# Kernel optimization log

Hardware: AMD Instinct MI355X
Metric: run time of the kernel (lower is better)

The kernel has to match this reference:

```python
import jax, jax.numpy as jnp
import numpy as np

N = 100_000      # nodes
E = 1_600_000    # edges (before self loops)
IN = 128         # in_dim
HID = 64         # hidden_dim (per head)
HEADS = 2
NEG_SLOPE = 0.2  # PyG GATConv default negative_slope


def setup_inputs() -> dict:
    key = jax.random.key(0)
    k = jax.random.split(key, 6)
    x = jax.random.normal(k[0], (N, IN), jnp.float32)
    edge_index = jax.random.randint(k[1], (2, E), 0, N, dtype=jnp.int64)
    # GATConv linear (no bias in lin, bias added after aggregation in PyG)
    W = jax.random.normal(k[2], (IN, HEADS * HID), jnp.float32) * (1.0 / np.sqrt(IN))
    att_src = jax.random.normal(k[3], (HEADS, HID), jnp.float32) * 0.1
    att_dst = jax.random.normal(k[4], (HEADS, HID), jnp.float32) * 0.1
    bias = jnp.zeros((HEADS * HID,), jnp.float32)
    prelu_w = jnp.full((HEADS * HID,), 0.25, jnp.float32)  # nn.PReLU default init
    return {"x": x, "edge_index": edge_index, "W": W, "att_src": att_src,
            "att_dst": att_dst, "bias": bias, "prelu_w": prelu_w}


def reference(x, edge_index, W, att_src, att_dst, bias, prelu_w):
    n = x.shape[0]
    h = (x @ W).reshape(n, HEADS, HID)                 # [N,H,C]
    a_s = jnp.einsum('nhc,hc->nh', h, att_src)         # [N,H]
    a_d = jnp.einsum('nhc,hc->nh', h, att_dst)         # [N,H]
    # add self loops (PyG default add_self_loops=True)
    loops = jnp.arange(n, dtype=edge_index.dtype)
    src = jnp.concatenate([edge_index[0], loops])      # [Et]
    dst = jnp.concatenate([edge_index[1], loops])      # [Et]
    logits = a_s[src] + a_d[dst]                       # [Et,H]
    logits = jnp.where(logits >= 0, logits, NEG_SLOPE * logits)  # LeakyReLU
    # segment softmax over destination neighborhoods
    m = jax.ops.segment_max(logits, dst, num_segments=n)         # [N,H]
    e = jnp.exp(logits - m[dst])
    s = jax.ops.segment_sum(e, dst, num_segments=n)              # [N,H]
    alpha = e / (s[dst] + 1e-16)                                 # [Et,H]
    # (attention dropout p=0.2 is identity in eval mode)
    msg = h[src] * alpha[..., None]                    # [Et,H,C]
    out = jax.ops.segment_sum(msg, dst, num_segments=n).reshape(n, HEADS * HID)
    out = out + bias
    # PReLU with per-channel weight
    return jnp.where(out >= 0, out, prelu_w * out)
```

## Files before the change

### kernel.cpp

```cpp
#include <hip/hip_runtime.h>
#include <hip/hip_fp16.h>
#include <cstdint>
#include <cstddef>

#define NEG_SLOPE 0.2f
#define BSH 8
#define BNODES 256
#define CAP 5120

typedef __attribute__((ext_vector_type(8))) short short8v;
typedef __attribute__((ext_vector_type(4))) float f32x4;
typedef __attribute__((ext_vector_type(2))) uint32_t u32x2;

__device__ __forceinline__ uint32_t bf16pair(float a, float b) {
    uint32_t ua = __float_as_uint(a), ub = __float_as_uint(b);
    ua = (ua + 0x7fffu + ((ua >> 16) & 1u)) >> 16;
    ub = (ub + 0x7fffu + ((ub >> 16) & 1u)) >> 16;
    return ua | (ub << 16);
}
__device__ __forceinline__ uint16_t rne16(float f) {
    uint32_t u = __float_as_uint(f);
    return (uint16_t)((u + 0x7fffu + ((u >> 16) & 1u)) >> 16);
}
__device__ __forceinline__ float bflo(uint32_t u) { return __uint_as_float(u << 16); }
__device__ __forceinline__ float bfhi(uint32_t u) { return __uint_as_float(u & 0xffff0000u); }
__device__ __forceinline__ uint32_t packf16(float a, float b) {
    __half2 h = __floats2half2_rn(a, b);
    return *reinterpret_cast<uint32_t*>(&h);
}

__global__ __launch_bounds__(256, 3) void gemm_att(
    const float* __restrict__ x, const float* __restrict__ W,
    const float* __restrict__ att_src, const float* __restrict__ att_dst,
    uint32_t* __restrict__ hb, float* __restrict__ a_s, float* __restrict__ a_d,
    int* __restrict__ gcur, int nb, int n)
{
    constexpr int PW = 136;
    __shared__ unsigned short Wt[128 * PW];
    __shared__ unsigned short Hs[4][16 * PW];
    const int tid  = threadIdx.x;
    const int w    = tid >> 6;
    const int lane = tid & 63;
    const int cl   = lane & 15;
    const int gq   = lane >> 4;
    const int base = blockIdx.x * 64;

    if (blockIdx.x == 0)
        for (int i = tid; i < nb; i += 256) gcur[i] = 0;

    const float4* W4 = (const float4*)W;
#pragma unroll
    for (int i = 0; i < 16; ++i) {
        int idx = tid + i * 256;
        int k = idx >> 5, c0 = (idx & 31) * 4;
        float4 v = W4[idx];
        Wt[(c0 + 0) * PW + k] = rne16(v.x);
        Wt[(c0 + 1) * PW + k] = rne16(v.y);
        Wt[(c0 + 2) * PW + k] = rne16(v.z);
        Wt[(c0 + 3) * PW + k] = rne16(v.w);
    }

    float asr[8], adr[8];
#pragma unroll
    for (int t = 0; t < 8; ++t) {
        asr[t] = att_src[t * 16 + cl];
        adr[t] = att_dst[t * 16 + cl];
    }
    __syncthreads();

    const int rowg = base + w * 16 + cl;
    const int rowc = rowg < n ? rowg : (n - 1);
    const f32x4* xp = (const f32x4*)(x + (size_t)rowc * 128);

    f32x4 acc[8];
#pragma unroll
    for (int t = 0; t < 8; ++t) acc[t] = (f32x4){0.f, 0.f, 0.f, 0.f};

#pragma unroll
    for (int s = 0; s < 4; ++s) {
        int kq = s * 8 + gq * 2;
        f32x4 f0 = __builtin_nontemporal_load(xp + kq);
        f32x4 f1 = __builtin_nontemporal_load(xp + kq + 1);
        union { short8v v; uint32_t d[4]; } A;
        A.d[0] = bf16pair(f0.x, f0.y);
        A.d[1] = bf16pair(f0.z, f0.w);
        A.d[2] = bf16pair(f1.x, f1.y);
        A.d[3] = bf16pair(f1.z, f1.w);
#pragma unroll
        for (int t = 0; t < 8; ++t) {
            union { short8v v; uint4 q; } B;
            B.q = *(const uint4*)&Wt[(t * 16 + cl) * PW + s * 32 + gq * 8];
            acc[t] = __builtin_amdgcn_mfma_f32_16x16x32_bf16(A.v, B.v, acc[t], 0, 0, 0);
        }
    }

    float ps0[4], ps1[4], pd0[4], pd1[4];
#pragma unroll
    for (int r = 0; r < 4; ++r) { ps0[r] = ps1[r] = pd0[r] = pd1[r] = 0.f; }
#pragma unroll
    for (int t = 0; t < 8; ++t) {
#pragma unroll
        for (int r = 0; r < 4; ++r) {
            float v = acc[t][r];
            if (t < 4) { ps0[r] = fmaf(v, asr[t], ps0[r]); pd0[r] = fmaf(v, adr[t], pd0[r]); }
            else       { ps1[r] = fmaf(v, asr[t], ps1[r]); pd1[r] = fmaf(v, adr[t], pd1[r]); }
        }
    }
#pragma unroll
    for (int off = 1; off < 16; off <<= 1) {
#pragma unroll
        for (int r = 0; r < 4; ++r) {
            ps0[r] += __shfl_xor(ps0[r], off);
            ps1[r] += __shfl_xor(ps1[r], off);
            pd0[r] += __shfl_xor(pd0[r], off);
            pd1[r] += __shfl_xor(pd1[r], off);
        }
    }
    if (cl == 0) {
#pragma unroll
        for (int r = 0; r < 4; ++r) {
            int rg = base + w * 16 + gq * 4 + r;
            if (rg < n) {
                a_s[rg * 2 + 0] = ps0[r]; a_s[rg * 2 + 1] = ps1[r];
                a_d[rg * 2 + 0] = pd0[r]; a_d[rg * 2 + 1] = pd1[r];
            }
        }
    }

#pragma unroll
    for (int t = 0; t < 8; ++t) {
#pragma unroll
        for (int r = 0; r < 4; ++r) {
            int row = gq * 4 + r;
            Hs[w][row * PW + t * 16 + cl] = rne16(acc[t][r]);
        }
    }
    __syncthreads();
#pragma unroll
    for (int q = 0; q < 4; ++q) {
        int row = q * 4 + gq;
        int cu  = 4 * cl;
        uint4 v = *(const uint4*)&Hs[w][row * PW + cu * 2];
        int rg = base + w * 16 + row;
        if (rg < n) *(uint4*)&hb[(size_t)rg * 64 + cu] = v;
    }
}

__global__ __launch_bounds__(256) void bucket_scatter(
    const int* __restrict__ src, const int* __restrict__ dst,
    int* __restrict__ gcur, uint32_t* __restrict__ pairs, int e, int nb)
{
    __shared__ int histL[512];
    __shared__ int gbaseL[512];
    const int tid = threadIdx.x;
    const int t0  = blockIdx.x * 4096;

    for (int i = tid; i < nb; i += 256) histL[i] = 0;
    __syncthreads();

    int      myb[16];
    int      myslot[16];
    uint32_t mypk[16];
#pragma unroll 16
    for (int k = 0; k < 16; ++k) {
        int i = t0 + tid + k * 256;
        if (i < e) {
            int s = __builtin_nontemporal_load(src + i);
            int d = __builtin_nontemporal_load(dst + i);
            int b = d >> BSH;
            myb[k]    = b;
            mypk[k]   = (uint32_t)s | ((uint32_t)(d & (BNODES - 1)) << 17);
            myslot[k] = atomicAdd(&histL[b], 1);
        } else myb[k] = -1;
    }
    __syncthreads();
    for (int i = tid; i < nb; i += 256) {
        int c = histL[i];
        gbaseL[i] = c ? atomicAdd(&gcur[i], c) : 0;
    }
    __syncthreads();
#pragma unroll 16
    for (int k = 0; k < 16; ++k) {
        if (myb[k] >= 0) {
            int p = gbaseL[myb[k]] + myslot[k];
            if (p < CAP) pairs[(size_t)myb[k] * CAP + p] = mypk[k];
        }
    }
}

__global__ __launch_bounds__(512) void build_csr(
    const uint32_t* __restrict__ pairs, const int* __restrict__ gcur,
    const float* __restrict__ a_s, const float* __restrict__ a_d,
    uint4* __restrict__ meta, uint2* __restrict__ edges, int n, int nb)
{
    __shared__ uint32_t pl[CAP];
    __shared__ int degL[BNODES], curL[BNODES];
    __shared__ float sumL[BNODES * 2];
    __shared__ float adL[BNODES * 2];
    __shared__ int bscan[512];
    __shared__ int wsum8[8];
    const int b = blockIdx.x, tid = threadIdx.x;
    const int lane = tid & 63, wid = tid >> 6;
    const int nbase = b * BNODES;
    const int nodes = min(BNODES, n - nbase);

    int tot = 0;
    if (tid < nb) {
        int nn = min(BNODES, n - tid * BNODES);
        tot = min(gcur[tid], CAP) + nn;
    }
    int sc = tot;
#pragma unroll
    for (int off = 1; off < 64; off <<= 1) {
        int t = __shfl_up(sc, off);
        if (lane >= off) sc += t;
    }
    if (lane == 63) wsum8[wid] = sc;
    __syncthreads();
    {
        int woff = 0;
#pragma unroll
        for (int k = 0; k < 8; ++k) woff += (k < wid) ? wsum8[k] : 0;
        bscan[tid] = sc + woff;
    }
    if (tid < BNODES) degL[tid] = 1;
    float es0 = 0.f, es1 = 0.f;
    if (tid < nodes) {
        int g = nbase + tid;
        float2 ad = ((const float2*)a_d)[g];
        adL[2 * tid]     = ad.x;
        adL[2 * tid + 1] = ad.y;
        float2 as = ((const float2*)a_s)[g];
        float l0 = as.x + ad.x; l0 = l0 >= 0.f ? l0 : NEG_SLOPE * l0;
        float l1 = as.y + ad.y; l1 = l1 >= 0.f ? l1 : NEG_SLOPE * l1;
        es0 = __expf(l0); es1 = __expf(l1);
        sumL[2 * tid] = es0; sumL[2 * tid + 1] = es1;
    }
    __syncthreads();
    const int C    = min(gcur[b], CAP);
    const int base = bscan[b] - (C + nodes);

    for (int i = tid; i < C; i += 512) {
        uint32_t p = __builtin_nontemporal_load(pairs + (size_t)b * CAP + i);
        pl[i] = p;
        atomicAdd(&degL[p >> 17], 1);
    }
    __syncthreads();

    int v = (tid < nodes) ? degL[tid] : 0;
    int sc2 = v;
#pragma unroll
    for (int off = 1; off < 64; off <<= 1) {
        int t = __shfl_up(sc2, off);
        if (lane >= off) sc2 += t;
    }
    if (lane == 63 && tid < BNODES) wsum8[wid] = sc2;
    __syncthreads();
    int woff2 = 0;
#pragma unroll
    for (int k = 0; k < 4; ++k) woff2 += (k < wid) ? wsum8[k] : 0;
    const int exc = sc2 - v + woff2;

    if (tid < nodes) {
        edges[base + exc] = make_uint2((uint32_t)(nbase + tid), packf16(es0, es1));
        curL[tid] = exc + 1;
    }
    __syncthreads();
    for (int i = tid; i < C; i += 512) {
        uint32_t p  = pl[i];
        int dl  = p >> 17;
        int s   = p & 0x1FFFF;
        float2 as = ((const float2*)a_s)[s];
        float l0 = as.x + adL[2 * dl];     l0 = l0 >= 0.f ? l0 : NEG_SLOPE * l0;
        float l1 = as.y + adL[2 * dl + 1]; l1 = l1 >= 0.f ? l1 : NEG_SLOPE * l1;
        float e0 = __expf(l0), e1 = __expf(l1);
        int pos = atomicAdd(&curL[dl], 1);
        edges[base + pos] = make_uint2((uint32_t)s, packf16(e0, e1));
        atomicAdd(&sumL[2 * dl],     e0);
        atomicAdd(&sumL[2 * dl + 1], e1);
    }
    __syncthreads();
    if (tid < nodes) {
        uint4 m;
        m.x = (uint32_t)(base + exc);
        m.y = (uint32_t)v;
        m.z = __float_as_uint(1.f / (sumL[2 * tid]     + 1e-16f));
        m.w = __float_as_uint(1.f / (sumL[2 * tid + 1] + 1e-16f));
        meta[nbase + tid] = m;
    }
}

__global__ __launch_bounds__(256) void attn_agg(
    const uint32_t* __restrict__ hb, const uint2* __restrict__ edges,
    const uint4* __restrict__ meta,
    const float* __restrict__ bias, const float* __restrict__ prelu_w,
    float* __restrict__ out, int n)
{
    const int gw   = (blockIdx.x * blockDim.x + threadIdx.x) >> 6;
    const int lane = threadIdx.x & 63;
    if (gw >= n) return;
    const uint4 mt  = meta[gw];
    const int start = (int)mt.x;
    const int deg   = (int)mt.y;
    const float inv0 = __uint_as_float(mt.z);
    const float inv1 = __uint_as_float(mt.w);

    if (deg <= 64) {
        int sv = 0; float al0 = 0.f, al1 = 0.f;
        if (lane < deg) {
            u32x2 ed = __builtin_nontemporal_load((const u32x2*)(edges + start + lane));
            sv = (int)ed.x;
            uint32_t ey = ed.y;
            __half2 h2 = *reinterpret_cast<__half2*>(&ey);
            al0 = __half2float(__low2half(h2))  * inv0;
            al1 = __half2float(__high2half(h2)) * inv1;
        }
        const int g = lane >> 4, r = lane & 15;
        float acc[8];
#pragma unroll
        for (int q = 0; q < 8; ++q) acc[q] = 0.f;

        const uint4* hb4 = (const uint4*)hb;
        const int iters = (deg + 15) >> 4;
        for (int jj = 0; jj < iters; ++jj) {
            const int j0 = jj * 16 + g;
            int   s0  = __shfl(sv, j0);
            int   s1  = __shfl(sv, j0 + 4);
            int   s2  = __shfl(sv, j0 + 8);
            int   s3  = __shfl(sv, j0 + 12);
            float A00 = __shfl(al0, j0),      A10 = __shfl(al1, j0);
            float A01 = __shfl(al0, j0 + 4),  A11 = __shfl(al1, j0 + 4);
            float A02 = __shfl(al0, j0 + 8),  A12 = __shfl(al1, j0 + 8);
            float A03 = __shfl(al0, j0 + 12), A13 = __shfl(al1, j0 + 12);
            float Aa = (r < 8) ? A00 : A10;
            float Ab = (r < 8) ? A01 : A11;
            float Ac = (r < 8) ? A02 : A12;
            float Ad = (r < 8) ? A03 : A13;
            uint4 qa = hb4[(size_t)s0 * 16 + r];
            uint4 qb = hb4[(size_t)s1 * 16 + r];
            uint4 qc = hb4[(size_t)s2 * 16 + r];
            uint4 qd = hb4[(size_t)s3 * 16 + r];
            acc[0] = fmaf(Aa, bflo(qa.x), acc[0]); acc[1] = fmaf(Aa, bfhi(qa.x), acc[1]);
            acc[2] = fmaf(Aa, bflo(qa.y), acc[2]); acc[3] = fmaf(Aa, bfhi(qa.y), acc[3]);
            acc[4] = fmaf(Aa, bflo(qa.z), acc[4]); acc[5] = fmaf(Aa, bfhi(qa.z), acc[5]);
            acc[6] = fmaf(Aa, bflo(qa.w), acc[6]); acc[7] = fmaf(Aa, bfhi(qa.w), acc[7]);
            acc[0] = fmaf(Ab, bflo(qb.x), acc[0]); acc[1] = fmaf(Ab, bfhi(qb.x), acc[1]);
            acc[2] = fmaf(Ab, bflo(qb.y), acc[2]); acc[3] = fmaf(Ab, bfhi(qb.y), acc[3]);
            acc[4] = fmaf(Ab, bflo(qb.z), acc[4]); acc[5] = fmaf(Ab, bfhi(qb.z), acc[5]);
            acc[6] = fmaf(Ab, bflo(qb.w), acc[6]); acc[7] = fmaf(Ab, bfhi(qb.w), acc[7]);
            acc[0] = fmaf(Ac, bflo(qc.x), acc[0]); acc[1] = fmaf(Ac, bfhi(qc.x), acc[1]);
            acc[2] = fmaf(Ac, bflo(qc.y), acc[2]); acc[3] = fmaf(Ac, bfhi(qc.y), acc[3]);
            acc[4] = fmaf(Ac, bflo(qc.z), acc[4]); acc[5] = fmaf(Ac, bfhi(qc.z), acc[5]);
            acc[6] = fmaf(Ac, bflo(qc.w), acc[6]); acc[7] = fmaf(Ac, bfhi(qc.w), acc[7]);
            acc[0] = fmaf(Ad, bflo(qd.x), acc[0]); acc[1] = fmaf(Ad, bfhi(qd.x), acc[1]);
            acc[2] = fmaf(Ad, bflo(qd.y), acc[2]); acc[3] = fmaf(Ad, bfhi(qd.y), acc[3]);
            acc[4] = fmaf(Ad, bflo(qd.z), acc[4]); acc[5] = fmaf(Ad, bfhi(qd.z), acc[5]);
            acc[6] = fmaf(Ad, bflo(qd.w), acc[6]); acc[7] = fmaf(Ad, bfhi(qd.w), acc[7]);
        }
#pragma unroll
        for (int q = 0; q < 8; ++q) {
            acc[q] += __shfl_xor(acc[q], 16);
            acc[q] += __shfl_xor(acc[q], 32);
        }
        if (lane < 16) {
            float4 b0 = ((const float4*)bias)[lane * 2];
            float4 b1 = ((const float4*)bias)[lane * 2 + 1];
            float4 p0 = ((const float4*)prelu_w)[lane * 2];
            float4 p1 = ((const float4*)prelu_w)[lane * 2 + 1];
            f32x4 w0, w1;
            w0.x = acc[0] + b0.x; w0.x = w0.x >= 0.f ? w0.x : p0.x * w0.x;
            w0.y = acc[1] + b0.y; w0.y = w0.y >= 0.f ? w0.y : p0.y * w0.y;
            w0.z = acc[2] + b0.z; w0.z = w0.z >= 0.f ? w0.z : p0.z * w0.z;
            w0.w = acc[3] + b0.w; w0.w = w0.w >= 0.f ? w0.w : p0.w * w0.w;
            w1.x = acc[4] + b1.x; w1.x = w1.x >= 0.f ? w1.x : p1.x * w1.x;
            w1.y = acc[5] + b1.y; w1.y = w1.y >= 0.f ? w1.y : p1.y * w1.y;
            w1.z = acc[6] + b1.z; w1.z = w1.z >= 0.f ? w1.z : p1.z * w1.z;
            w1.w = acc[7] + b1.w; w1.w = w1.w >= 0.f ? w1.w : p1.w * w1.w;
            float* op = out + (size_t)gw * 128 + lane * 8;
            __builtin_nontemporal_store(w0, (f32x4*)op);
            __builtin_nontemporal_store(w1, (f32x4*)(op + 4));
        }
    } else {
        float accL = 0.f, accH = 0.f;
        for (int t0 = 0; t0 < deg; t0 += 64) {
            int tt = t0 + lane;
            int sv = 0; float al0 = 0.f, al1 = 0.f;
            if (tt < deg) {
                uint2 ed = edges[start + tt];
                sv = (int)ed.x;
                __half2 h2 = *reinterpret_cast<__half2*>(&ed.y);
                al0 = __half2float(__low2half(h2))  * inv0;
                al1 = __half2float(__high2half(h2)) * inv1;
            }
            int kmax = min(64, deg - t0);
            for (int j = 0; j < kmax; ++j) {
                int   s  = __shfl(sv, j);
                float A0 = __shfl(al0, j);
                float A1 = __shfl(al1, j);
                float A  = (lane < 32) ? A0 : A1;
                uint32_t u = hb[(size_t)s * 64 + lane];
                accL = fmaf(A, bflo(u), accL);
                accH = fmaf(A, bfhi(u), accH);
            }
        }
        float2 bz = ((const float2*)bias)[lane];
        float2 pw = ((const float2*)prelu_w)[lane];
        float o0 = accL + bz.x, o1 = accH + bz.y;
        o0 = o0 >= 0.f ? o0 : pw.x * o0;
        o1 = o1 >= 0.f ? o1 : pw.y * o1;
        float2 rr; rr.x = o0; rr.y = o1;
        ((float2*)out)[(size_t)gw * 64 + lane] = rr;
    }
}

extern "C" void kernel_launch(void* const* d_in, const int* in_sizes, int n_in,
                              void* d_out, int out_size, void* d_ws, size_t ws_size,
                              hipStream_t stream)
{
    const float* x        = (const float*)d_in[0];
    const int*   ei       = (const int*)d_in[1];
    const float* W        = (const float*)d_in[2];
    const float* att_src  = (const float*)d_in[3];
    const float* att_dst  = (const float*)d_in[4];
    const float* bias     = (const float*)d_in[5];
    const float* prelu_w  = (const float*)d_in[6];
    float* out = (float*)d_out;

    const int n = in_sizes[0] / 128;
    const int e = in_sizes[1] / 2;
    const int* srcp = ei;
    const int* dstp = ei + e;
    const int nb = (n + BNODES - 1) / BNODES;

    uint32_t* hb    = (uint32_t*)d_ws;
    uint4*    meta  = (uint4*)(hb + (size_t)n * 64);
    float*    a_s   = (float*)(meta + n);
    float*    a_d   = a_s + (size_t)n * 2;
    int*      gcur  = (int*)(a_d + (size_t)n * 2);
    uint32_t* pairs = (uint32_t*)(gcur + 512);
    uint2*    edges = (uint2*)(pairs + (size_t)nb * CAP);

    gemm_att<<<(n + 63) / 64, 256, 0, stream>>>(x, W, att_src, att_dst,
                                                hb, a_s, a_d, gcur, nb, n);
    bucket_scatter<<<(e + 4095) / 4096, 256, 0, stream>>>(srcp, dstp, gcur, pairs, e, nb);
    build_csr<<<nb, 512, 0, stream>>>(pairs, gcur, a_s, a_d, meta, edges, n, nb);
    attn_agg<<<(n + 3) / 4, 256, 0, stream>>>(hb, edges, meta, bias, prelu_w, out, n);
}
```

Baseline: 160.5 us.

## Merge GEMM and edge bucket scatter into one launch; specialize aggregation by degree

```diff
diff --git a/kernel.cpp b/kernel.cpp
--- a/kernel.cpp
+++ b/kernel.cpp
@@ -29,24 +29,64 @@
     return *reinterpret_cast<uint32_t*>(&h);
 }
 
-__global__ __launch_bounds__(256, 3) void gemm_att(
+__global__ __launch_bounds__(256, 3) void gemm_scatter(
     const float* __restrict__ x, const float* __restrict__ W,
     const float* __restrict__ att_src, const float* __restrict__ att_dst,
     uint32_t* __restrict__ hb, float* __restrict__ a_s, float* __restrict__ a_d,
-    int* __restrict__ gcur, int nb, int n)
+    const int* __restrict__ src, const int* __restrict__ dst,
+    int* __restrict__ gcur, uint32_t* __restrict__ pairs,
+    int e, int nb, int n, int nbs)
 {
     constexpr int PW = 136;
-    __shared__ unsigned short Wt[128 * PW];
-    __shared__ unsigned short Hs[4][16 * PW];
-    const int tid  = threadIdx.x;
+    __shared__ __align__(16) char smem[52224];
+    const int tid = threadIdx.x;
+
+    if (blockIdx.x < nbs) {
+        int* histL  = (int*)smem;
+        int* gbaseL = histL + 512;
+        const int t0 = blockIdx.x * 4096;
+
+        for (int i = tid; i < nb; i += 256) histL[i] = 0;
+        __syncthreads();
+
+        int      myb[16];
+        int      myslot[16];
+        uint32_t mypk[16];
+#pragma unroll 16
+        for (int k = 0; k < 16; ++k) {
+            int i = t0 + tid + k * 256;
+            if (i < e) {
+                int s = __builtin_nontemporal_load(src + i);
+                int d = __builtin_nontemporal_load(dst + i);
+                int b = d >> BSH;
+                myb[k]    = b;
+                mypk[k]   = (uint32_t)s | ((uint32_t)(d & (BNODES - 1)) << 17);
+                myslot[k] = atomicAdd(&histL[b], 1);
+            } else myb[k] = -1;
+        }
+        __syncthreads();
+        for (int i = tid; i < nb; i += 256) {
+            int c = histL[i];
+            gbaseL[i] = c ? atomicAdd(&gcur[i], c) : 0;
+        }
+        __syncthreads();
+#pragma unroll 16
+        for (int k = 0; k < 16; ++k) {
+            if (myb[k] >= 0) {
+                int p = gbaseL[myb[k]] + myslot[k];
+                if (p < CAP) pairs[(size_t)myb[k] * CAP + p] = mypk[k];
+            }
+        }
+        return;
+    }
+
+    unsigned short* Wt = (unsigned short*)smem;
+    unsigned short* Hs = (unsigned short*)(smem + 34816);
     const int w    = tid >> 6;
     const int lane = tid & 63;
     const int cl   = lane & 15;
     const int gq   = lane >> 4;
-    const int base = blockIdx.x * 64;
-
-    if (blockIdx.x == 0)
-        for (int i = tid; i < nb; i += 256) gcur[i] = 0;
+    const int base = (blockIdx.x - nbs) * 64;
 
     const float4* W4 = (const float4*)W;
 #pragma unroll
@@ -132,7 +172,7 @@
 #pragma unroll
         for (int r = 0; r < 4; ++r) {
             int row = gq * 4 + r;
-            Hs[w][row * PW + t * 16 + cl] = rne16(acc[t][r]);
+            Hs[(size_t)w * 16 * PW + row * PW + t * 16 + cl] = rne16(acc[t][r]);
         }
     }
     __syncthreads();
@@ -140,51 +180,9 @@
     for (int q = 0; q < 4; ++q) {
         int row = q * 4 + gq;
         int cu  = 4 * cl;
-        uint4 v = *(const uint4*)&Hs[w][row * PW + cu * 2];
+        uint4 v = *(const uint4*)&Hs[(size_t)w * 16 * PW + row * PW + cu * 2];
         int rg = base + w * 16 + row;
         if (rg < n) *(uint4*)&hb[(size_t)rg * 64 + cu] = v;
-    }
-}
-
-__global__ __launch_bounds__(256) void bucket_scatter(
-    const int* __restrict__ src, const int* __restrict__ dst,
-    int* __restrict__ gcur, uint32_t* __restrict__ pairs, int e, int nb)
-{
-    __shared__ int histL[512];
-    __shared__ int gbaseL[512];
-    const int tid = threadIdx.x;
-    const int t0  = blockIdx.x * 4096;
-
-    for (int i = tid; i < nb; i += 256) histL[i] = 0;
-    __syncthreads();
-
-    int      myb[16];
-    int      myslot[16];
-    uint32_t mypk[16];
-#pragma unroll 16
-    for (int k = 0; k < 16; ++k) {
-        int i = t0 + tid + k * 256;
-        if (i < e) {
-            int s = __builtin_nontemporal_load(src + i);
-            int d = __builtin_nontemporal_load(dst + i);
-            int b = d >> BSH;
-            myb[k]    = b;
-            mypk[k]   = (uint32_t)s | ((uint32_t)(d & (BNODES - 1)) << 17);
-            myslot[k] = atomicAdd(&histL[b], 1);
-        } else myb[k] = -1;
-    }
-    __syncthreads();
-    for (int i = tid; i < nb; i += 256) {
-        int c = histL[i];
-        gbaseL[i] = c ? atomicAdd(&gcur[i], c) : 0;
-    }
-    __syncthreads();
-#pragma unroll 16
-    for (int k = 0; k < 16; ++k) {
-        if (myb[k] >= 0) {
-            int p = gbaseL[myb[k]] + myslot[k];
-            if (p < CAP) pairs[(size_t)myb[k] * CAP + p] = mypk[k];
-        }
     }
 }
 
@@ -319,43 +317,74 @@
         float acc[8];
 #pragma unroll
         for (int q = 0; q < 8; ++q) acc[q] = 0.f;
-
         const uint4* hb4 = (const uint4*)hb;
-        const int iters = (deg + 15) >> 4;
-        for (int jj = 0; jj < iters; ++jj) {
-            const int j0 = jj * 16 + g;
-            int   s0  = __shfl(sv, j0);
-            int   s1  = __shfl(sv, j0 + 4);
-            int   s2  = __shfl(sv, j0 + 8);
-            int   s3  = __shfl(sv, j0 + 12);
-            float A00 = __shfl(al0, j0),      A10 = __shfl(al1, j0);
-            float A01 = __shfl(al0, j0 + 4),  A11 = __shfl(al1, j0 + 4);
-            float A02 = __shfl(al0, j0 + 8),  A12 = __shfl(al1, j0 + 8);
-            float A03 = __shfl(al0, j0 + 12), A13 = __shfl(al1, j0 + 12);
-            float Aa = (r < 8) ? A00 : A10;
-            float Ab = (r < 8) ? A01 : A11;
-            float Ac = (r < 8) ? A02 : A12;
-            float Ad = (r < 8) ? A03 : A13;
-            uint4 qa = hb4[(size_t)s0 * 16 + r];
-            uint4 qb = hb4[(size_t)s1 * 16 + r];
-            uint4 qc = hb4[(size_t)s2 * 16 + r];
-            uint4 qd = hb4[(size_t)s3 * 16 + r];
-            acc[0] = fmaf(Aa, bflo(qa.x), acc[0]); acc[1] = fmaf(Aa, bfhi(qa.x), acc[1]);
-            acc[2] = fmaf(Aa, bflo(qa.y), acc[2]); acc[3] = fmaf(Aa, bfhi(qa.y), acc[3]);
-            acc[4] = fmaf(Aa, bflo(qa.z), acc[4]); acc[5] = fmaf(Aa, bfhi(qa.z), acc[5]);
-            acc[6] = fmaf(Aa, bflo(qa.w), acc[6]); acc[7] = fmaf(Aa, bfhi(qa.w), acc[7]);
-            acc[0] = fmaf(Ab, bflo(qb.x), acc[0]); acc[1] = fmaf(Ab, bfhi(qb.x), acc[1]);
-            acc[2] = fmaf(Ab, bflo(qb.y), acc[2]); acc[3] = fmaf(Ab, bfhi(qb.y), acc[3]);
-            acc[4] = fmaf(Ab, bflo(qb.z), acc[4]); acc[5] = fmaf(Ab, bfhi(qb.z), acc[5]);
-            acc[6] = fmaf(Ab, bflo(qb.w), acc[6]); acc[7] = fmaf(Ab, bfhi(qb.w), acc[7]);
-            acc[0] = fmaf(Ac, bflo(qc.x), acc[0]); acc[1] = fmaf(Ac, bfhi(qc.x), acc[1]);
-            acc[2] = fmaf(Ac, bflo(qc.y), acc[2]); acc[3] = fmaf(Ac, bfhi(qc.y), acc[3]);
-            acc[4] = fmaf(Ac, bflo(qc.z), acc[4]); acc[5] = fmaf(Ac, bfhi(qc.z), acc[5]);
-            acc[6] = fmaf(Ac, bflo(qc.w), acc[6]); acc[7] = fmaf(Ac, bfhi(qc.w), acc[7]);
-            acc[0] = fmaf(Ad, bflo(qd.x), acc[0]); acc[1] = fmaf(Ad, bfhi(qd.x), acc[1]);
-            acc[2] = fmaf(Ad, bflo(qd.y), acc[2]); acc[3] = fmaf(Ad, bfhi(qd.y), acc[3]);
-            acc[4] = fmaf(Ad, bflo(qd.z), acc[4]); acc[5] = fmaf(Ad, bfhi(qd.z), acc[5]);
-            acc[6] = fmaf(Ad, bflo(qd.w), acc[6]); acc[7] = fmaf(Ad, bfhi(qd.w), acc[7]);
+
+        if (deg <= 16) {
+            float Aj[4]; uint4 q[4];
+#pragma unroll
+            for (int k = 0; k < 4; ++k) {
+                int j = g + 4 * k;
+                int s = __shfl(sv, j);
+                float A0 = __shfl(al0, j), A1 = __shfl(al1, j);
+                Aj[k] = (r < 8) ? A0 : A1;
+                q[k] = hb4[(size_t)s * 16 + r];
+            }
+#pragma unroll
+            for (int k = 0; k < 4; ++k) {
+                acc[0] = fmaf(Aj[k], bflo(q[k].x), acc[0]);
+                acc[1] = fmaf(Aj[k], bfhi(q[k].x), acc[1]);
+                acc[2] = fmaf(Aj[k], bflo(q[k].y), acc[2]);
+                acc[3] = fmaf(Aj[k], bfhi(q[k].y), acc[3]);
+                acc[4] = fmaf(Aj[k], bflo(q[k].z), acc[4]);
+                acc[5] = fmaf(Aj[k], bfhi(q[k].z), acc[5]);
+                acc[6] = fmaf(Aj[k], bflo(q[k].w), acc[6]);
+                acc[7] = fmaf(Aj[k], bfhi(q[k].w), acc[7]);
+            }
+        } else if (deg <= 32) {
+            float Aj[8]; uint4 q[8];
+#pragma unroll
+            for (int k = 0; k < 8; ++k) {
+                int j = g + 4 * k;
+                int s = __shfl(sv, j);
+                float A0 = __shfl(al0, j), A1 = __shfl(al1, j);
+                Aj[k] = (r < 8) ? A0 : A1;
+                q[k] = hb4[(size_t)s * 16 + r];
+            }
+#pragma unroll
+            for (int k = 0; k < 8; ++k) {
+                acc[0] = fmaf(Aj[k], bflo(q[k].x), acc[0]);
+                acc[1] = fmaf(Aj[k], bfhi(q[k].x), acc[1]);
+                acc[2] = fmaf(Aj[k], bflo(q[k].y), acc[2]);
+                acc[3] = fmaf(Aj[k], bfhi(q[k].y), acc[3]);
+                acc[4] = fmaf(Aj[k], bflo(q[k].z), acc[4]);
+                acc[5] = fmaf(Aj[k], bfhi(q[k].z), acc[5]);
+                acc[6] = fmaf(Aj[k], bflo(q[k].w), acc[6]);
+                acc[7] = fmaf(Aj[k], bfhi(q[k].w), acc[7]);
+            }
+        } else {
+            const int iters = (deg + 15) >> 4;
+            for (int jj = 0; jj < iters; ++jj) {
+                float Aj[4]; uint4 q[4];
+#pragma unroll
+                for (int k = 0; k < 4; ++k) {
+                    int j = jj * 16 + g + 4 * k;
+                    int s = __shfl(sv, j);
+                    float A0 = __shfl(al0, j), A1 = __shfl(al1, j);
+                    Aj[k] = (r < 8) ? A0 : A1;
+                    q[k] = hb4[(size_t)s * 16 + r];
+                }
+#pragma unroll
+                for (int k = 0; k < 4; ++k) {
+                    acc[0] = fmaf(Aj[k], bflo(q[k].x), acc[0]);
+                    acc[1] = fmaf(Aj[k], bfhi(q[k].x), acc[1]);
+                    acc[2] = fmaf(Aj[k], bflo(q[k].y), acc[2]);
+                    acc[3] = fmaf(Aj[k], bfhi(q[k].y), acc[3]);
+                    acc[4] = fmaf(Aj[k], bflo(q[k].z), acc[4]);
+                    acc[5] = fmaf(Aj[k], bfhi(q[k].z), acc[5]);
+                    acc[6] = fmaf(Aj[k], bflo(q[k].w), acc[6]);
+                    acc[7] = fmaf(Aj[k], bfhi(q[k].w), acc[7]);
+                }
+            }
         }
 #pragma unroll
         for (int q = 0; q < 8; ++q) {
@@ -430,7 +459,9 @@
     const int e = in_sizes[1] / 2;
     const int* srcp = ei;
     const int* dstp = ei + e;
-    const int nb = (n + BNODES - 1) / BNODES;
+    const int nb  = (n + BNODES - 1) / BNODES;
+    const int nbs = (e + 4095) / 4096;
+    const int nbg = (n + 63) / 64;
 
     uint32_t* hb    = (uint32_t*)d_ws;
     uint4*    meta  = (uint4*)(hb + (size_t)n * 64);
@@ -440,9 +471,10 @@
     uint32_t* pairs = (uint32_t*)(gcur + 512);
     uint2*    edges = (uint2*)(pairs + (size_t)nb * CAP);
 
-    gemm_att<<<(n + 63) / 64, 256, 0, stream>>>(x, W, att_src, att_dst,
-                                                hb, a_s, a_d, gcur, nb, n);
-    bucket_scatter<<<(e + 4095) / 4096, 256, 0, stream>>>(srcp, dstp, gcur, pairs, e, nb);
+    hipMemsetAsync(gcur, 0, 512 * sizeof(int), stream);
+    gemm_scatter<<<nbs + nbg, 256, 0, stream>>>(x, W, att_src, att_dst,
+                                                hb, a_s, a_d, srcp, dstp,
+                                                gcur, pairs, e, nb, n, nbs);
     build_csr<<<nb, 512, 0, stream>>>(pairs, gcur, a_s, a_d, meta, edges, n, nb);
     attn_agg<<<(n + 3) / 4, 256, 0, stream>>>(hb, edges, meta, bias, prelu_w, out, n);
 }
```

Measured after the change: 159.3 us. No clear change (-0.7%).

## Merge GEMM and edge bucket-scatter into one launch with block-range dispatch

Applied to the files above, without the earlier changes.

```diff
diff --git a/kernel.cpp b/kernel.cpp
--- a/kernel.cpp
+++ b/kernel.cpp
@@ -29,24 +29,64 @@
     return *reinterpret_cast<uint32_t*>(&h);
 }
 
-__global__ __launch_bounds__(256, 3) void gemm_att(
+__global__ __launch_bounds__(256, 3) void gemm_scatter(
     const float* __restrict__ x, const float* __restrict__ W,
     const float* __restrict__ att_src, const float* __restrict__ att_dst,
     uint32_t* __restrict__ hb, float* __restrict__ a_s, float* __restrict__ a_d,
-    int* __restrict__ gcur, int nb, int n)
+    const int* __restrict__ src, const int* __restrict__ dst,
+    int* __restrict__ gcur, uint32_t* __restrict__ pairs,
+    int e, int nb, int n, int nbs)
 {
     constexpr int PW = 136;
-    __shared__ unsigned short Wt[128 * PW];
-    __shared__ unsigned short Hs[4][16 * PW];
-    const int tid  = threadIdx.x;
+    __shared__ __align__(16) char smem[52224];
+    const int tid = threadIdx.x;
+
+    if (blockIdx.x < nbs) {
+        int* histL  = (int*)smem;
+        int* gbaseL = histL + 512;
+        const int t0 = blockIdx.x * 4096;
+
+        for (int i = tid; i < nb; i += 256) histL[i] = 0;
+        __syncthreads();
+
+        int      myb[16];
+        int      myslot[16];
+        uint32_t mypk[16];
+#pragma unroll 16
+        for (int k = 0; k < 16; ++k) {
+            int i = t0 + tid + k * 256;
+            if (i < e) {
+                int s = __builtin_nontemporal_load(src + i);
+                int d = __builtin_nontemporal_load(dst + i);
+                int b = d >> BSH;
+                myb[k]    = b;
+                mypk[k]   = (uint32_t)s | ((uint32_t)(d & (BNODES - 1)) << 17);
+                myslot[k] = atomicAdd(&histL[b], 1);
+            } else myb[k] = -1;
+        }
+        __syncthreads();
+        for (int i = tid; i < nb; i += 256) {
+            int c = histL[i];
+            gbaseL[i] = c ? atomicAdd(&gcur[i], c) : 0;
+        }
+        __syncthreads();
+#pragma unroll 16
+        for (int k = 0; k < 16; ++k) {
+            if (myb[k] >= 0) {
+                int p = gbaseL[myb[k]] + myslot[k];
+                if (p < CAP) pairs[(size_t)myb[k] * CAP + p] = mypk[k];
+            }
+        }
+        return;
+    }
+
+    unsigned short* Wt = (unsigned short*)smem;
+    unsigned short* Hs = (unsigned short*)(smem + 34816);
     const int w    = tid >> 6;
     const int lane = tid & 63;
     const int cl   = lane & 15;
     const int gq   = lane >> 4;
-    const int base = blockIdx.x * 64;
-
-    if (blockIdx.x == 0)
-        for (int i = tid; i < nb; i += 256) gcur[i] = 0;
+    const int base = (blockIdx.x - nbs) * 64;
 
     const float4* W4 = (const float4*)W;
 #pragma unroll
@@ -132,7 +172,7 @@
 #pragma unroll
         for (int r = 0; r < 4; ++r) {
             int row = gq * 4 + r;
-            Hs[w][row * PW + t * 16 + cl] = rne16(acc[t][r]);
+            Hs[(size_t)w * 16 * PW + row * PW + t * 16 + cl] = rne16(acc[t][r]);
         }
     }
     __syncthreads();
@@ -140,51 +180,9 @@
     for (int q = 0; q < 4; ++q) {
         int row = q * 4 + gq;
         int cu  = 4 * cl;
-        uint4 v = *(const uint4*)&Hs[w][row * PW + cu * 2];
+        uint4 v = *(const uint4*)&Hs[(size_t)w * 16 * PW + row * PW + cu * 2];
         int rg = base + w * 16 + row;
         if (rg < n) *(uint4*)&hb[(size_t)rg * 64 + cu] = v;
-    }
-}
-
-__global__ __launch_bounds__(256) void bucket_scatter(
-    const int* __restrict__ src, const int* __restrict__ dst,
-    int* __restrict__ gcur, uint32_t* __restrict__ pairs, int e, int nb)
-{
-    __shared__ int histL[512];
-    __shared__ int gbaseL[512];
-    const int tid = threadIdx.x;
-    const int t0  = blockIdx.x * 4096;
-
-    for (int i = tid; i < nb; i += 256) histL[i] = 0;
-    __syncthreads();
-
-    int      myb[16];
-    int      myslot[16];
-    uint32_t mypk[16];
-#pragma unroll 16
-    for (int k = 0; k < 16; ++k) {
-        int i = t0 + tid + k * 256;
-        if (i < e) {
-            int s = __builtin_nontemporal_load(src + i);
-            int d = __builtin_nontemporal_load(dst + i);
-            int b = d >> BSH;
-            myb[k]    = b;
-            mypk[k]   = (uint32_t)s | ((uint32_t)(d & (BNODES - 1)) << 17);
-            myslot[k] = atomicAdd(&histL[b], 1);
-        } else myb[k] = -1;
-    }
-    __syncthreads();
-    for (int i = tid; i < nb; i += 256) {
-        int c = histL[i];
-        gbaseL[i] = c ? atomicAdd(&gcur[i], c) : 0;
-    }
-    __syncthreads();
-#pragma unroll 16
-    for (int k = 0; k < 16; ++k) {
-        if (myb[k] >= 0) {
-            int p = gbaseL[myb[k]] + myslot[k];
-            if (p < CAP) pairs[(size_t)myb[k] * CAP + p] = mypk[k];
-        }
     }
 }
 
@@ -430,7 +428,9 @@
     const int e = in_sizes[1] / 2;
     const int* srcp = ei;
     const int* dstp = ei + e;
-    const int nb = (n + BNODES - 1) / BNODES;
+    const int nb  = (n + BNODES - 1) / BNODES;
+    const int nbs = (e + 4095) / 4096;
+    const int nbg = (n + 63) / 64;
 
     uint32_t* hb    = (uint32_t*)d_ws;
     uint4*    meta  = (uint4*)(hb + (size_t)n * 64);
@@ -440,9 +440,10 @@
     uint32_t* pairs = (uint32_t*)(gcur + 512);
     uint2*    edges = (uint2*)(pairs + (size_t)nb * CAP);
 
-    gemm_att<<<(n + 63) / 64, 256, 0, stream>>>(x, W, att_src, att_dst,
-                                                hb, a_s, a_d, gcur, nb, n);
-    bucket_scatter<<<(e + 4095) / 4096, 256, 0, stream>>>(srcp, dstp, gcur, pairs, e, nb);
+    hipMemsetAsync(gcur, 0, 512 * sizeof(int), stream);
+    gemm_scatter<<<nbs + nbg, 256, 0, stream>>>(x, W, att_src, att_dst,
+                                                hb, a_s, a_d, srcp, dstp,
+                                                gcur, pairs, e, nb, n, nbs);
     build_csr<<<nb, 512, 0, stream>>>(pairs, gcur, a_s, a_d, meta, edges, n, nb);
     attn_agg<<<(n + 3) / 4, 256, 0, stream>>>(hb, edges, meta, bias, prelu_w, out, n);
 }
```

Measured after the change: 153.9 us. 1.04x faster.
